# Optimization experiments

Measured on AMD Instinct MI355X. Metric: run time of the kernel, lower is better.

## Reference

```python
import jax, jax.numpy as jnp
import numpy as np

EPS = 1e-5

def _conv(x, w, pad, groups=1):
    return jax.lax.conv_general_dilated(
        x, w, window_strides=(1, 1), padding=[(pad, pad), (pad, pad)],
        dimension_numbers=('NCHW', 'OIHW', 'NCHW'), feature_group_count=groups)

def _bn(x, g, b, m, v):
    # inference batch-norm, per-channel
    s = g * jax.lax.rsqrt(v + EPS)
    return x * s[None, :, None, None] + (b - m * s)[None, :, None, None]

def setup_inputs() -> dict:
    key = jax.random.key(0)
    ks = jax.random.split(key, 20)
    B, C, H, W = 32, 128, 64, 64
    cs = C // 2  # c_split = 64
    d = {
        'x': jax.random.normal(ks[0], (B, C, H, W), jnp.float32),
        'weights': jax.random.uniform(ks[1], (B, 2), jnp.float32),
        'indices': jax.random.randint(ks[2], (B, 2), 0, 4, jnp.int32),
        # expert 0: Conv(cs -> C, k=3, p=1) + BN + SiLU
        'e0_w': jax.random.normal(ks[3], (C, cs, 3, 3), jnp.float32) * 0.05,
        'e0_g': jax.random.uniform(ks[4], (C,), jnp.float32, 0.5, 1.5),
        'e0_b': jax.random.normal(ks[5], (C,), jnp.float32) * 0.1,
        'e0_m': jax.random.normal(ks[6], (C,), jnp.float32) * 0.1,
        'e0_v': jax.random.uniform(ks[7], (C,), jnp.float32, 0.5, 1.5),
        # expert 1: depthwise 5x5 (cs, groups=cs) -> 1x1 (cs -> C) -> BN -> SiLU
        'e1_dw': jax.random.normal(ks[8], (cs, 1, 5, 5), jnp.float32) * 0.05,
        'e1_pw': jax.random.normal(ks[9], (C, cs, 1, 1), jnp.float32) * 0.05,
        'e1_g': jax.random.uniform(ks[10], (C,), jnp.float32, 0.5, 1.5),
        'e1_b': jax.random.normal(ks[11], (C,), jnp.float32) * 0.1,
        'e1_m': jax.random.normal(ks[12], (C,), jnp.float32) * 0.1,
        'e1_v': jax.random.uniform(ks[13], (C,), jnp.float32, 0.5, 1.5),
        # expert 2: GhostConv(C -> C): cv1 = Conv(C, C//2, 3), cv2 = Conv(C//2, C//2, 5, groups=C//2)
        'e2a_w': jax.random.normal(ks[14], (cs, C, 3, 3), jnp.float32) * 0.05,
        'e2a_g': jax.random.uniform(ks[15], (cs,), jnp.float32, 0.5, 1.5),
        'e2a_b': jax.random.normal(ks[16], (cs,), jnp.float32) * 0.1,
        'e2a_m': jax.random.normal(ks[17], (cs,), jnp.float32) * 0.1,
        'e2a_v': jax.random.uniform(ks[18], (cs,), jnp.float32, 0.5, 1.5),
        'e2b_w': jax.random.normal(ks[19], (cs, 1, 5, 5), jnp.float32) * 0.05,
    }
    ks2 = jax.random.split(jax.random.key(1), 4)
    d['e2b_g'] = jax.random.uniform(ks2[0], (cs,), jnp.float32, 0.5, 1.5)
    d['e2b_b'] = jax.random.normal(ks2[1], (cs,), jnp.float32) * 0.1
    d['e2b_m'] = jax.random.normal(ks2[2], (cs,), jnp.float32) * 0.1
    d['e2b_v'] = jax.random.uniform(ks2[3], (cs,), jnp.float32, 0.5, 1.5)
    return d

def _forward(x, weights, indices,
             e0_w, e0_g, e0_b, e0_m, e0_v,
             e1_dw, e1_pw, e1_g, e1_b, e1_m, e1_v,
             e2a_w, e2a_g, e2a_b, e2a_m, e2a_v,
             e2b_w, e2b_g, e2b_b, e2b_m, e2b_v):
    C = x.shape[1]
    cs = C // 2
    x_rgb, x_ir = x[:, :cs], x[:, cs:]
    # expert outputs computed densely over the whole batch, masked combine below
    e0 = jax.nn.silu(_bn(_conv(x_rgb, e0_w, pad=1), e0_g, e0_b, e0_m, e0_v))
    e1 = jax.nn.silu(_bn(_conv(_conv(x_ir, e1_dw, pad=2, groups=cs), e1_pw, pad=0),
                         e1_g, e1_b, e1_m, e1_v))
    g1 = jax.nn.silu(_bn(_conv(x, e2a_w, pad=1), e2a_g, e2a_b, e2a_m, e2a_v))
    g2 = jax.nn.silu(_bn(_conv(g1, e2b_w, pad=2, groups=cs), e2b_g, e2b_b, e2b_m, e2b_v))
    e2 = jnp.concatenate([g1, g2], axis=1)
    out = jnp.zeros_like(x)
    K = indices.shape[1]
    for k in range(K):  # small fixed top-k loop
        idx = indices[:, k][:, None, None, None]          # [B,1,1,1]
        w = weights[:, k][:, None, None, None]            # [B,1,1,1]
        out = out + jnp.where(idx == 0, e0 * w, 0.0)
        out = out + jnp.where(idx == 1, e1 * w, 0.0)
        out = out + jnp.where(idx == 2, e2 * w, 0.0)
        out = out + jnp.where(idx == 3, x * 0.1, 0.0)
    return out

def reference(x, weights, indices,
              e0_w, e0_g, e0_b, e0_m, e0_v,
              e1_dw, e1_pw, e1_g, e1_b, e1_m, e1_v,
              e2a_w, e2a_g, e2a_b, e2a_m, e2a_v,
              e2b_w, e2b_g, e2b_b, e2b_m, e2b_v):
    return _forward(x, weights, indices,
                    e0_w, e0_g, e0_b, e0_m, e0_v,
                    e1_dw, e1_pw, e1_g, e1_b, e1_m, e1_v,
                    e2a_w, e2a_g, e2a_b, e2a_m, e2a_v,
                    e2b_w, e2b_g, e2b_b, e2b_m, e2b_v)
```

## Files before the change

kernel.cpp:

```cpp
#include <hip/hip_runtime.h>

#define B_  32
#define C_  128
#define CS  64
#define H_  64
#define W_  64
#define HW  (H_*W_)

typedef __attribute__((ext_vector_type(8))) short bf16x8_t;
typedef __attribute__((ext_vector_type(4))) float f32x4_t;
typedef unsigned short u16;
typedef unsigned int   u32;

__device__ __forceinline__ float silu_f(float v) { return v / (1.f + __expf(-v)); }

__device__ __forceinline__ u16 f2bf(float f) {
    u32 u = __float_as_uint(f);
    u = (u + 0x7FFFu + ((u >> 16) & 1u)) >> 16;
    return (u16)u;
}
__device__ __forceinline__ float bf2f(u16 u) {
    return __uint_as_float(((u32)u) << 16);
}
__device__ __forceinline__ u32 pack2(float a, float b) {
    return (u32)f2bf(a) | ((u32)f2bf(b) << 16);
}

__device__ __forceinline__ void get_coeffs(const float* __restrict__ wts,
                                           const int* __restrict__ idxs, int b,
                                           float& c0, float& c1, float& c2, float& cid) {
    int   i0 = idxs[b*2+0], i1 = idxs[b*2+1];
    float w0 = wts[b*2+0],  w1 = wts[b*2+1];
    c0  = (i0==0?w0:0.f)   + (i1==0?w1:0.f);
    c1  = (i0==1?w0:0.f)   + (i1==1?w1:0.f);
    c2  = (i0==2?w0:0.f)   + (i1==2?w1:0.f);
    cid = (i0==3?0.1f:0.f) + (i1==3?0.1f:0.f);
}

__global__ __launch_bounds__(256) void k_prep(
    const float* __restrict__ e0w, const float* __restrict__ e2aw, const float* __restrict__ e1pw,
    u16* __restrict__ Wt0f, u16* __restrict__ Wt2f, u16* __restrict__ Wt1f)
{
    const int i0 = blockIdx.x*256 + threadIdx.x, stride = gridDim.x*256;
    for (int i = i0; i < 73728; i += stride) {
        int j = i&7, lane = (i>>3)&63, cog = (i>>9)&7, kc = (i>>12)&1, tap = i>>13;
        int co = cog*16 + (lane&15), ci = kc*32 + (lane>>4)*8 + j;
        Wt0f[i] = f2bf(e0w[(size_t)(co*64 + ci)*9 + tap]);
    }
    for (int i = i0; i < 73728; i += stride) {
        int j = i&7, lane = (i>>3)&63, cog = (i>>9)&3, kc = (i>>11)&3, tap = i>>13;
        int co = cog*16 + (lane&15), ci = kc*32 + (lane>>4)*8 + j;
        Wt2f[i] = f2bf(e2aw[(size_t)(co*128 + ci)*9 + tap]);
    }
    for (int i = i0; i < 8192; i += stride) {
        int j = i&7, lane = (i>>3)&63, cog = (i>>9)&7, kc = (i>>12)&1;
        int co = cog*16 + (lane&15), ci = kc*32 + (lane>>4)*8 + j;
        Wt1f[i] = f2bf(e1pw[(size_t)co*64 + ci]);
    }
}

__global__ __launch_bounds__(256) void k_to_nhwc(
    const float* __restrict__ x, const float* __restrict__ wts, const int* __restrict__ idxs,
    u16* __restrict__ xhA, u16* __restrict__ xhB)
{
    const int b = blockIdx.y, h = blockIdx.x, t = threadIdx.x;
    float c0, c1, c2, cid;
    get_coeffs(wts, idxs, b, c0, c1, c2, cid);
    if (c0 == 0.f && c2 == 0.f) return;
    const int np = (c2 != 0.f) ? 2 : 1;
    const int chmax = np*64;

    __shared__ float ld[128*66];
    for (int i = t; i < chmax*16; i += 256) {
        int ch = i >> 4, q = i & 15;
        float4 v = *(const float4*)(x + ((size_t)(b*C_+ch))*HW + h*64 + q*4);
        float* p = &ld[ch*66 + q*4];
        p[0] = v.x; p[1] = v.y; p[2] = v.z; p[3] = v.w;
    }
    __syncthreads();

    const int px = t >> 2, sub = t & 3;
    const size_t base64 = ((size_t)(b*66 + h+1)*66 + (px+1))*64;
    for (int c = sub; c < chmax/8; c += 4) {
        uint4 v;
        u32 w[4];
        #pragma unroll
        for (int k = 0; k < 4; ++k)
            w[k] = pack2(ld[(c*8 + 2*k)*66 + px], ld[(c*8 + 2*k + 1)*66 + px]);
        v.x = w[0]; v.y = w[1]; v.z = w[2]; v.w = w[3];
        u16* dst = (c < 8) ? (xhA + base64 + c*8) : (xhB + base64 + (c-8)*8);
        *(uint4*)dst = v;
    }
    for (int i = t; i < 16*np; i += 256) {
        int pl = i >> 4, j = i & 15;
        int col = (j >> 3)*65, cg = j & 7;
        u16* ph = pl ? xhB : xhA;
        uint4 z; z.x = z.y = z.z = z.w = 0u;
        *(uint4*)(ph + ((size_t)(b*66 + h+1)*66 + col)*64 + cg*8) = z;
    }
    if (h == 0 || h == 63) {
        int r = (h == 0) ? 0 : 65;
        for (int i = t; i < 66*8*np; i += 256) {
            int pl = i / (66*8), j = i % (66*8);
            int col = j >> 3, cg = j & 7;
            u16* ph = pl ? xhB : xhA;
            uint4 z; z.x = z.y = z.z = z.w = 0u;
            *(uint4*)(ph + ((size_t)(b*66 + r)*64*66/64*64 + (size_t)col*64) + cg*8) = z;
        }
    }
}

template<int MODE>
__device__ __forceinline__ void conv_body(
    u16* lin, const u16* __restrict__ xhA, const u16* __restrict__ xhB,
    const float* __restrict__ x, const u16* __restrict__ Wtf,
    const float* __restrict__ gg, const float* __restrict__ bbn,
    const float* __restrict__ mm, const float* __restrict__ vv,
    float* __restrict__ out, u16* __restrict__ g1,
    int b, int orow0, int t, float cexp, float cid)
{
    constexpr int NPL  = (MODE == 0) ? 1 : 2;
    constexpr int NCF  = (MODE == 0) ? 4 : 2;
    constexpr int COUT = (MODE == 0) ? 128 : 64;
    constexpr int KCT  = (MODE == 0) ? 2 : 4;
    constexpr int NIT  = 9*KCT;

    const size_t src0 = ((size_t)(b*66 + orow0))*66*64;
    #pragma unroll
    for (int pl = 0; pl < NPL; ++pl) {
        const u16* sp = (pl ? xhB : xhA) + src0;
        char* lp = ((char*)lin) + pl*33792;
        for (int d = t*16; d < 33792; d += 4096) {
            u32 s = (u32)d ^ ((((u32)d >> 7) & 7u) << 4);
            *(uint4*)(lp + d) = *(const uint4*)((const char*)sp + s);
        }
    }
    __syncthreads();

    const int lane = t & 63, l15 = lane & 15, kg = lane >> 4;
    const int wv = t >> 6, cw = wv >> 1, rw = wv & 1;
    const int cobase = cw * (NCF*16);
    const int row = orow0 + rw;

    f32x4_t acc[NCF][4];
    #pragma unroll
    for (int cf = 0; cf < NCF; ++cf)
        #pragma unroll
        for (int pf = 0; pf < 4; ++pf)
            acc[cf][pf] = (f32x4_t){0.f, 0.f, 0.f, 0.f};

    const u16* wb = Wtf + (size_t)(cobase >> 4)*512 + (size_t)lane*8;

    bf16x8_t aC[NCF], aN[NCF];
    auto loadA = [&](int it, bf16x8_t* a) {
        const u16* wt = wb + (size_t)(it*(COUT/16))*512;
        #pragma unroll
        for (int cf = 0; cf < NCF; ++cf)
            a[cf] = *(const bf16x8_t*)(wt + (cf << 9));
    };
    auto ldsB = [&](int it, int pf) -> bf16x8_t {
        const int tap = it / KCT, kcg = it % KCT;
        const int pl = (MODE == 0) ? 0 : (kcg >> 1);
        const int kc = (MODE == 0) ? kcg : (kcg & 1);
        const int dh = tap / 3, dwp = tap % 3;
        const int p  = (rw + dh)*66 + pf*16 + l15 + dwp;
        u32 a = (u32)p*128 + (u32)kc*64 + (u32)kg*16;
        a ^= ((u32)(p & 7)) << 4;
        return *(const bf16x8_t*)(((const char*)lin) + pl*33792 + a);
    };

    loadA(0, aC);
    #pragma unroll
    for (int it = 0; it < NIT; ++it) {
        bf16x8_t* ac = (it & 1) ? aN : aC;
        bf16x8_t* an = (it & 1) ? aC : aN;
        if (it + 1 < NIT) loadA(it + 1, an);
        bf16x8_t bfr[4];
        #pragma unroll
        for (int pf = 0; pf < 4; ++pf) bfr[pf] = ldsB(it, pf);
        #pragma unroll
        for (int pf = 0; pf < 4; ++pf)
            #pragma unroll
            for (int cf = 0; cf < NCF; ++cf)
                acc[cf][pf] = __builtin_amdgcn_mfma_f32_16x16x32_bf16(ac[cf], bfr[pf], acc[cf][pf], 0, 0, 0);
    }

    #pragma unroll
    for (int cf = 0; cf < NCF; ++cf) {
        float sarr[4], tarr[4];
        #pragma unroll
        for (int r = 0; r < 4; ++r) {
            int co = cobase + cf*16 + kg*4 + r;
            float s = gg[co] * rsqrtf(vv[co] + 1e-5f);
            sarr[r] = s; tarr[r] = bbn[co] - mm[co]*s;
        }
        #pragma unroll
        for (int pf = 0; pf < 4; ++pf) {
            int px = pf*16 + l15;
            size_t rowoff = (size_t)row*64 + px;
            #pragma unroll
            for (int r = 0; r < 4; ++r) {
                int co = cobase + cf*16 + kg*4 + r;
                float v = silu_f(acc[cf][pf][r]*sarr[r] + tarr[r]);
                if (MODE == 0) {
                    size_t o = ((size_t)(b*C_+co))*HW + rowoff;
                    float idv = (cid != 0.f) ? cid*x[o] : 0.f;
                    out[o] = cexp*v + idv;
                } else {
                    g1[((size_t)(b*CS+co))*HW + rowoff] = f2bf(v);
                }
            }
        }
    }
}

__global__ __launch_bounds__(256, 3) void k_conv(
    const u16* __restrict__ xhA, const u16* __restrict__ xhB, const float* __restrict__ x,
    const float* __restrict__ wts, const int* __restrict__ idxs,
    const u16* __restrict__ Wt0f, const u16* __restrict__ Wt2f,
    const float* __restrict__ e0g, const float* __restrict__ e0b,
    const float* __restrict__ e0m, const float* __restrict__ e0v,
    const float* __restrict__ e2ag, const float* __restrict__ e2ab,
    const float* __restrict__ e2am, const float* __restrict__ e2av,
    float* __restrict__ out, u16* __restrict__ g1)
{
    __shared__ u16 lin[2*16896];
    const int b = blockIdx.y, bx = blockIdx.x, t = threadIdx.x;
    float c0, c1, c2, cid;
    get_coeffs(wts, idxs, b, c0, c1, c2, cid);

    if (bx < 32) {
        const int orow0 = bx*2;
        if (c0 == 0.f) {
            for (int i = t; i < 4096; i += 256) {
                int q = i & 15, r = (i >> 4) & 1, ch = i >> 5;
                size_t o = ((size_t)(b*C_+ch))*HW + (size_t)(orow0+r)*64 + q*4;
                float4 ov;
                if (cid != 0.f) {
                    float4 xv = *(const float4*)(x + o);
                    ov.x = cid*xv.x; ov.y = cid*xv.y; ov.z = cid*xv.z; ov.w = cid*xv.w;
                } else { ov.x = ov.y = ov.z = ov.w = 0.f; }
                *(float4*)(out + o) = ov;
            }
            return;
        }
        conv_body<0>(lin, xhA, xhB, x, Wt0f, e0g, e0b, e0m, e0v, out, nullptr,
                     b, orow0, t, c0, cid);
    } else {
        if (c2 == 0.f) return;
        conv_body<1>(lin, xhA, xhB, x, Wt2f, e2ag, e2ab, e2am, e2av, nullptr, g1,
                     b, (bx-32)*2, t, c2, 0.f);
    }
}

__global__ __launch_bounds__(256) void k_e1(
    const float* __restrict__ x, const float* __restrict__ wts, const int* __restrict__ idxs,
    const float* __restrict__ dww, const u16* __restrict__ Wt1f,
    const float* __restrict__ gg, const float* __restrict__ bb,
    const float* __restrict__ mm, const float* __restrict__ vv,
    float* __restrict__ out)
{
    const int b = blockIdx.y, band = blockIdx.x, t = threadIdx.x;
    const int orow0 = band*2;

    float c0, c1, c2, cid;
    get_coeffs(wts, idxs, b, c0, c1, c2, cid);
    if (c1 == 0.f) return;

    __shared__ u16  lin[6*64*70];
    __shared__ u16  lout[128*72];
    __shared__ float wl[64*26];

    for (int i = t; i < 64*25; i += 256) wl[(i/25)*26 + (i%25)] = dww[i];
    for (int i = t; i < 6*64*16; i += 256) {
        int q = i & 15, ch = (i >> 4) & 63, r = i >> 10;
        int hh = orow0 - 2 + r;
        u32 w0 = 0u, w1 = 0u;
        if (hh >= 0 && hh < H_) {
            float4 v = *(const float4*)(x + ((size_t)(b*C_ + CS + ch))*HW + hh*64 + q*4);
            w0 = pack2(v.x, v.y); w1 = pack2(v.z, v.w);
        }
        u32* dst = (u32*)&lin[(r*64 + ch)*70 + 2 + q*4];
        dst[0] = w0; dst[1] = w1;
    }
    for (int i = t; i < 6*64; i += 256) {
        int ch = i & 63, r = i >> 6;
        *(u32*)&lin[(r*64 + ch)*70]      = 0u;
        u32* e = (u32*)&lin[(r*64 + ch)*70 + 66];
        e[0] = 0u; e[1] = 0u;
    }
    __syncthreads();

    const int lane = t & 63, chl = lane & 15, cs = lane >> 4;
    const int wv = t >> 6, outrow = wv & 1, chhalf = wv >> 1;

    #pragma unroll
    for (int chi = 0; chi < 2; ++chi) {
        const int ch = chhalf*32 + chl + chi*16;
        const float* wch = &wl[ch*26];
        float accp[16];
        #pragma unroll
        for (int p = 0; p < 16; ++p) accp[p] = 0.f;
        #pragma unroll
        for (int kh = 0; kh < 5; ++kh) {
            const u16* src = &lin[((outrow + kh)*64 + ch)*70 + cs*16];
            float rb[20];
            #pragma unroll
            for (int k = 0; k < 10; ++k) {
                u32 u = *(const u32*)(src + 2*k);
                rb[2*k]   = __uint_as_float(u << 16);
                rb[2*k+1] = __uint_as_float(u & 0xFFFF0000u);
            }
            #pragma unroll
            for (int kw = 0; kw < 5; ++kw) {
                float wvv = wch[kh*5 + kw];
                #pragma unroll
                for (int p = 0; p < 16; ++p) accp[p] += rb[p+kw]*wvv;
            }
        }
        const int px0 = outrow*64 + cs*16;
        #pragma unroll
        for (int p = 0; p < 16; ++p) lout[(px0+p)*72 + ch] = f2bf(accp[p]);
    }
    __syncthreads();

    const int l15 = lane & 15, kg = lane >> 4;
    const int cw = wv >> 1, pwv = wv & 1;
    f32x4_t acc[4][4];
    #pragma unroll
    for (int cf = 0; cf < 4; ++cf)
        #pragma unroll
        for (int pf = 0; pf < 4; ++pf)
            acc[cf][pf] = (f32x4_t){0.f, 0.f, 0.f, 0.f};

    #pragma unroll
    for (int kc = 0; kc < 2; ++kc) {
        const u16* wt = Wt1f + (((size_t)(kc*8 + cw*4)) << 9) + lane*8;
        bf16x8_t af[4];
        #pragma unroll
        for (int cf = 0; cf < 4; ++cf) af[cf] = *(const bf16x8_t*)(wt + (cf << 9));
        const int k0 = kc*32 + kg*8;
        #pragma unroll
        for (int pf = 0; pf < 4; ++pf) {
            bf16x8_t bfr = *(const bf16x8_t*)&lout[(pwv*64 + pf*16 + l15)*72 + k0];
            #pragma unroll
            for (int cf = 0; cf < 4; ++cf)
                acc[cf][pf] = __builtin_amdgcn_mfma_f32_16x16x32_bf16(af[cf], bfr, acc[cf][pf], 0, 0, 0);
        }
    }

    #pragma unroll
    for (int cf = 0; cf < 4; ++cf) {
        float sarr[4], tarr[4];
        #pragma unroll
        for (int r = 0; r < 4; ++r) {
            int co = cw*64 + cf*16 + kg*4 + r;
            float s = gg[co] * rsqrtf(vv[co] + 1e-5f);
            sarr[r] = s; tarr[r] = bb[co] - mm[co]*s;
        }
        #pragma unroll
        for (int pf = 0; pf < 4; ++pf) {
            int px = pwv*64 + pf*16 + l15;
            size_t rowoff = (size_t)(orow0 + (px>>6))*64 + (px&63);
            #pragma unroll
            for (int r = 0; r < 4; ++r) {
                int co = cw*64 + cf*16 + kg*4 + r;
                float v = silu_f(acc[cf][pf][r]*sarr[r] + tarr[r]);
                out[((size_t)(b*C_+co))*HW + rowoff] += c1*v;
            }
        }
    }
}

__global__ __launch_bounds__(256) void k_e2b(
    const u16* __restrict__ g1, const float* __restrict__ wts, const int* __restrict__ idxs,
    const float* __restrict__ dww, const float* __restrict__ gg, const float* __restrict__ bb,
    const float* __restrict__ mm, const float* __restrict__ vv, float* __restrict__ out)
{
    const int b = blockIdx.y, band = blockIdx.x, t = threadIdx.x;
    const int orow0 = band*2;

    float c0, c1, c2, cid;
    get_coeffs(wts, idxs, b, c0, c1, c2, cid);
    if (c2 == 0.f) return;

    __shared__ u16  lin[6*64*70];
    __shared__ float wl[64*26];

    for (int i = t; i < 64*25; i += 256) wl[(i/25)*26 + (i%25)] = dww[i];
    for (int i = t; i < 6*64*16; i += 256) {
        int q = i & 15, ch = (i >> 4) & 63, r = i >> 10;
        int hh = orow0 - 2 + r;
        u32 w0 = 0u, w1 = 0u;
        if (hh >= 0 && hh < H_) {
            const u32* src = (const u32*)(g1 + ((size_t)(b*CS+ch))*HW + hh*64 + q*4);
            w0 = src[0]; w1 = src[1];
        }
        u32* dst = (u32*)&lin[(r*64 + ch)*70 + 2 + q*4];
        dst[0] = w0; dst[1] = w1;
    }
    for (int i = t; i < 6*64; i += 256) {
        int ch = i & 63, r = i >> 6;
        *(u32*)&lin[(r*64 + ch)*70] = 0u;
        u32* e = (u32*)&lin[(r*64 + ch)*70 + 66];
        e[0] = 0u; e[1] = 0u;
    }
    __syncthreads();

    for (int i = t; i < 2*64*16; i += 256) {
        int q = i & 15, ch = (i >> 4) & 63, r = i >> 10;
        const u16* src = &lin[((r+2)*64 + ch)*70 + 2 + q*4];
        float* op = out + ((size_t)(b*C_+ch))*HW + (size_t)(orow0+r)*64 + q*4;
        float4 ov = *(float4*)op;
        ov.x += c2*bf2f(src[0]); ov.y += c2*bf2f(src[1]);
        ov.z += c2*bf2f(src[2]); ov.w += c2*bf2f(src[3]);
        *(float4*)op = ov;
    }

    const int lane = t & 63, chl = lane & 15, cs = lane >> 4;
    const int wv = t >> 6, outrow = wv & 1, chhalf = wv >> 1;

    #pragma unroll
    for (int chi = 0; chi < 2; ++chi) {
        const int ch = chhalf*32 + chl + chi*16;
        const float* wch = &wl[ch*26];
        float accp[16];
        #pragma unroll
        for (int p = 0; p < 16; ++p) accp[p] = 0.f;
        #pragma unroll
        for (int kh = 0; kh < 5; ++kh) {
            const u16* src = &lin[((outrow + kh)*64 + ch)*70 + cs*16];
            float rb[20];
            #pragma unroll
            for (int k = 0; k < 10; ++k) {
                u32 u = *(const u32*)(src + 2*k);
                rb[2*k]   = __uint_as_float(u << 16);
                rb[2*k+1] = __uint_as_float(u & 0xFFFF0000u);
            }
            #pragma unroll
            for (int kw = 0; kw < 5; ++kw) {
                float wvv = wch[kh*5 + kw];
                #pragma unroll
                for (int p = 0; p < 16; ++p) accp[p] += rb[p+kw]*wvv;
            }
        }
        float s = gg[ch] * rsqrtf(vv[ch] + 1e-5f);
        float tt = bb[ch] - mm[ch]*s;
        float* op = out + ((size_t)(b*C_ + CS + ch))*HW + (size_t)(orow0+outrow)*64 + cs*16;
        #pragma unroll
        for (int q = 0; q < 4; ++q) {
            float4 ov = *(float4*)(op + q*4);
            ov.x += c2*silu_f(accp[q*4+0]*s + tt);
            ov.y += c2*silu_f(accp[q*4+1]*s + tt);
            ov.z += c2*silu_f(accp[q*4+2]*s + tt);
            ov.w += c2*silu_f(accp[q*4+3]*s + tt);
            *(float4*)(op + q*4) = ov;
        }
    }
}

extern "C" void kernel_launch(void* const* d_in, const int* in_sizes, int n_in,
                              void* d_out, int out_size, void* d_ws, size_t ws_size,
                              hipStream_t stream) {
    const float* x    = (const float*)d_in[0];
    const float* wts  = (const float*)d_in[1];
    const int*   idxs = (const int*)  d_in[2];
    const float* e0w  = (const float*)d_in[3];
    const float* e0g  = (const float*)d_in[4];
    const float* e0b  = (const float*)d_in[5];
    const float* e0m  = (const float*)d_in[6];
    const float* e0v  = (const float*)d_in[7];
    const float* e1dw = (const float*)d_in[8];
    const float* e1pw = (const float*)d_in[9];
    const float* e1g  = (const float*)d_in[10];
    const float* e1b  = (const float*)d_in[11];
    const float* e1m  = (const float*)d_in[12];
    const float* e1v  = (const float*)d_in[13];
    const float* e2aw = (const float*)d_in[14];
    const float* e2ag = (const float*)d_in[15];
    const float* e2ab = (const float*)d_in[16];
    const float* e2am = (const float*)d_in[17];
    const float* e2av = (const float*)d_in[18];
    const float* e2bw = (const float*)d_in[19];
    const float* e2bg = (const float*)d_in[20];
    const float* e2bb = (const float*)d_in[21];
    const float* e2bm = (const float*)d_in[22];
    const float* e2bv = (const float*)d_in[23];

    float* out = (float*)d_out;

    const size_t PLANE = (size_t)32*66*66*64;
    u16* xhA  = (u16*)d_ws;
    u16* xhB  = xhA + PLANE;
    u16* g1   = xhB + PLANE;
    u16* Wt0f = g1 + (size_t)8388608;
    u16* Wt2f = Wt0f + 73728;
    u16* Wt1f = Wt2f + 73728;

    k_prep<<<128, 256, 0, stream>>>(e0w, e2aw, e1pw, Wt0f, Wt2f, Wt1f);
    k_to_nhwc<<<dim3(64, B_), 256, 0, stream>>>(x, wts, idxs, xhA, xhB);
    k_conv<<<dim3(64, B_), 256, 0, stream>>>(
        xhA, xhB, x, wts, idxs, Wt0f, Wt2f,
        e0g, e0b, e0m, e0v, e2ag, e2ab, e2am, e2av, out, g1);
    k_e1<<<dim3(32, B_), 256, 0, stream>>>(
        x, wts, idxs, e1dw, Wt1f, e1g, e1b, e1m, e1v, out);
    k_e2b<<<dim3(32, B_), 256, 0, stream>>>(
        g1, wts, idxs, e2bw, e2bg, e2bb, e2bm, e2bv, out);
}
```

Baseline: 116.0 us.

## Merge expert-0 and GhostConv-cv1 convolutions into one block sharing staged input

Expert 0 and the GhostConv first conv previously ran in separate blocks that each staged the same input band into LDS. They now run in one block per two-row band: waves 0-1 compute the 128-channel expert-0 conv over both rows, and waves 2-3 compute the 64-channel cv1 conv, one row each. The change removes redundant global-to-LDS loads of the shared xhA plane and halves the grid. In exchange each wave holds more accumulators, occupancy drops to 2 blocks per SM, and the work is split unevenly between the two wave pairs. It also fixes the halo-row zero-fill address expression.

```diff
diff --git a/kernel.cpp b/kernel.cpp
--- a/kernel.cpp
+++ b/kernel.cpp
@@ -105,48 +105,27 @@
             int col = j >> 3, cg = j & 7;
             u16* ph = pl ? xhB : xhA;
             uint4 z; z.x = z.y = z.z = z.w = 0u;
-            *(uint4*)(ph + ((size_t)(b*66 + r)*64*66/64*64 + (size_t)col*64) + cg*8) = z;
-        }
-    }
-}
-
-template<int MODE>
-__device__ __forceinline__ void conv_body(
-    u16* lin, const u16* __restrict__ xhA, const u16* __restrict__ xhB,
-    const float* __restrict__ x, const u16* __restrict__ Wtf,
+            *(uint4*)(ph + ((size_t)(b*66 + r)*66 + (size_t)col)*64 + cg*8) = z;
+        }
+    }
+}
+
+template<int NCF, int NPF, int KCT, int COUT, int MODE>
+__device__ __forceinline__ void conv_wave(
+    const char* lin, const u16* __restrict__ Wtf,
     const float* __restrict__ gg, const float* __restrict__ bbn,
     const float* __restrict__ mm, const float* __restrict__ vv,
-    float* __restrict__ out, u16* __restrict__ g1,
-    int b, int orow0, int t, float cexp, float cid)
+    const float* __restrict__ x, float* __restrict__ out, u16* __restrict__ g1,
+    int b, int orow0, int rbase, int cobase, int lane, float cexp, float cid)
 {
-    constexpr int NPL  = (MODE == 0) ? 1 : 2;
-    constexpr int NCF  = (MODE == 0) ? 4 : 2;
-    constexpr int COUT = (MODE == 0) ? 128 : 64;
-    constexpr int KCT  = (MODE == 0) ? 2 : 4;
-    constexpr int NIT  = 9*KCT;
-
-    const size_t src0 = ((size_t)(b*66 + orow0))*66*64;
-    #pragma unroll
-    for (int pl = 0; pl < NPL; ++pl) {
-        const u16* sp = (pl ? xhB : xhA) + src0;
-        char* lp = ((char*)lin) + pl*33792;
-        for (int d = t*16; d < 33792; d += 4096) {
-            u32 s = (u32)d ^ ((((u32)d >> 7) & 7u) << 4);
-            *(uint4*)(lp + d) = *(const uint4*)((const char*)sp + s);
-        }
-    }
-    __syncthreads();
-
-    const int lane = t & 63, l15 = lane & 15, kg = lane >> 4;
-    const int wv = t >> 6, cw = wv >> 1, rw = wv & 1;
-    const int cobase = cw * (NCF*16);
-    const int row = orow0 + rw;
-
-    f32x4_t acc[NCF][4];
+    constexpr int NIT = 9*KCT;
+    const int l15 = lane & 15, kg = lane >> 4;
+
+    f32x4_t acc[NCF][NPF];
     #pragma unroll
     for (int cf = 0; cf < NCF; ++cf)
         #pragma unroll
-        for (int pf = 0; pf < 4; ++pf)
+        for (int pf = 0; pf < NPF; ++pf)
             acc[cf][pf] = (f32x4_t){0.f, 0.f, 0.f, 0.f};
 
     const u16* wb = Wtf + (size_t)(cobase >> 4)*512 + (size_t)lane*8;
@@ -160,13 +139,14 @@
     };
     auto ldsB = [&](int it, int pf) -> bf16x8_t {
         const int tap = it / KCT, kcg = it % KCT;
-        const int pl = (MODE == 0) ? 0 : (kcg >> 1);
-        const int kc = (MODE == 0) ? kcg : (kcg & 1);
+        const int pl = kcg >> 1, kc = kcg & 1;
         const int dh = tap / 3, dwp = tap % 3;
-        const int p  = (rw + dh)*66 + pf*16 + l15 + dwp;
+        const int prow = (NPF == 8) ? (pf >> 2) : rbase;
+        const int pcol = (NPF == 8) ? ((pf & 3)*16) : (pf*16);
+        const int p = (prow + dh)*66 + pcol + l15 + dwp;
         u32 a = (u32)p*128 + (u32)kc*64 + (u32)kg*16;
         a ^= ((u32)(p & 7)) << 4;
-        return *(const bf16x8_t*)(((const char*)lin) + pl*33792 + a);
+        return *(const bf16x8_t*)(lin + pl*33792 + a);
     };
 
     loadA(0, aC);
@@ -175,14 +155,13 @@
         bf16x8_t* ac = (it & 1) ? aN : aC;
         bf16x8_t* an = (it & 1) ? aC : aN;
         if (it + 1 < NIT) loadA(it + 1, an);
-        bf16x8_t bfr[4];
-        #pragma unroll
-        for (int pf = 0; pf < 4; ++pf) bfr[pf] = ldsB(it, pf);
-        #pragma unroll
-        for (int pf = 0; pf < 4; ++pf)
+        #pragma unroll
+        for (int pf = 0; pf < NPF; ++pf) {
+            bf16x8_t bfr = ldsB(it, pf);
             #pragma unroll
             for (int cf = 0; cf < NCF; ++cf)
-                acc[cf][pf] = __builtin_amdgcn_mfma_f32_16x16x32_bf16(ac[cf], bfr[pf], acc[cf][pf], 0, 0, 0);
+                acc[cf][pf] = __builtin_amdgcn_mfma_f32_16x16x32_bf16(ac[cf], bfr, acc[cf][pf], 0, 0, 0);
+        }
     }
 
     #pragma unroll
@@ -195,9 +174,10 @@
             sarr[r] = s; tarr[r] = bbn[co] - mm[co]*s;
         }
         #pragma unroll
-        for (int pf = 0; pf < 4; ++pf) {
-            int px = pf*16 + l15;
-            size_t rowoff = (size_t)row*64 + px;
+        for (int pf = 0; pf < NPF; ++pf) {
+            const int prow = (NPF == 8) ? (pf >> 2) : rbase;
+            const int pcol = (NPF == 8) ? ((pf & 3)*16) : (pf*16);
+            size_t rowoff = (size_t)(orow0 + prow)*64 + pcol + l15;
             #pragma unroll
             for (int r = 0; r < 4; ++r) {
                 int co = cobase + cf*16 + kg*4 + r;
@@ -214,7 +194,7 @@
     }
 }
 
-__global__ __launch_bounds__(256, 3) void k_conv(
+__global__ __launch_bounds__(256, 2) void k_conv(
     const u16* __restrict__ xhA, const u16* __restrict__ xhB, const float* __restrict__ x,
     const float* __restrict__ wts, const int* __restrict__ idxs,
     const u16* __restrict__ Wt0f, const u16* __restrict__ Wt2f,
@@ -224,17 +204,51 @@
     const float* __restrict__ e2am, const float* __restrict__ e2av,
     float* __restrict__ out, u16* __restrict__ g1)
 {
-    __shared__ u16 lin[2*16896];
-    const int b = blockIdx.y, bx = blockIdx.x, t = threadIdx.x;
+    __shared__ char lin[2*33792];
+    const int b = blockIdx.y, orow0 = blockIdx.x*2, t = threadIdx.x;
     float c0, c1, c2, cid;
     get_coeffs(wts, idxs, b, c0, c1, c2, cid);
-
-    if (bx < 32) {
-        const int orow0 = bx*2;
-        if (c0 == 0.f) {
-            for (int i = t; i < 4096; i += 256) {
-                int q = i & 15, r = (i >> 4) & 1, ch = i >> 5;
-                size_t o = ((size_t)(b*C_+ch))*HW + (size_t)(orow0+r)*64 + q*4;
+    const bool need0 = (c0 != 0.f), need2 = (c2 != 0.f);
+
+    if (!need0 && !need2) {
+        for (int i = t; i < 4096; i += 256) {
+            int ch = i >> 5, q = i & 31;
+            size_t o = ((size_t)(b*C_+ch))*HW + (size_t)orow0*64 + q*4;
+            float4 ov;
+            if (cid != 0.f) {
+                float4 xv = *(const float4*)(x + o);
+                ov.x = cid*xv.x; ov.y = cid*xv.y; ov.z = cid*xv.z; ov.w = cid*xv.w;
+            } else { ov.x = ov.y = ov.z = ov.w = 0.f; }
+            *(float4*)(out + o) = ov;
+        }
+        return;
+    }
+
+    {
+        const size_t src0 = ((size_t)(b*66 + orow0))*66*64;
+        for (int d = t*16; d < 33792; d += 4096) {
+            u32 s = (u32)d ^ ((((u32)d >> 7) & 7u) << 4);
+            *(uint4*)(lin + d) = *(const uint4*)((const char*)(xhA + src0) + s);
+        }
+        if (need2) {
+            for (int d = t*16; d < 33792; d += 4096) {
+                u32 s = (u32)d ^ ((((u32)d >> 7) & 7u) << 4);
+                *(uint4*)(lin + 33792 + d) = *(const uint4*)((const char*)(xhB + src0) + s);
+            }
+        }
+    }
+    __syncthreads();
+
+    const int wv = t >> 6, lane = t & 63;
+    if (wv < 2) {
+        if (need0) {
+            conv_wave<4, 8, 2, 128, 0>(lin, Wt0f, e0g, e0b, e0m, e0v, x, out, nullptr,
+                                       b, orow0, 0, wv*64, lane, c0, cid);
+        } else {
+            for (int k = 0; k < 32; ++k) {
+                int idx = k*64 + lane;
+                int ch = wv*64 + (idx >> 5), q = idx & 31;
+                size_t o = ((size_t)(b*C_+ch))*HW + (size_t)orow0*64 + q*4;
                 float4 ov;
                 if (cid != 0.f) {
                     float4 xv = *(const float4*)(x + o);
@@ -242,14 +256,11 @@
                 } else { ov.x = ov.y = ov.z = ov.w = 0.f; }
                 *(float4*)(out + o) = ov;
             }
-            return;
-        }
-        conv_body<0>(lin, xhA, xhB, x, Wt0f, e0g, e0b, e0m, e0v, out, nullptr,
-                     b, orow0, t, c0, cid);
+        }
     } else {
-        if (c2 == 0.f) return;
-        conv_body<1>(lin, xhA, xhB, x, Wt2f, e2ag, e2ab, e2am, e2av, nullptr, g1,
-                     b, (bx-32)*2, t, c2, 0.f);
+        if (need2)
+            conv_wave<4, 4, 4, 64, 1>(lin, Wt2f, e2ag, e2ab, e2am, e2av, x, nullptr, g1,
+                                      b, orow0, wv - 2, 0, lane, c2, 0.f);
     }
 }
 
@@ -499,7 +510,7 @@
 
     k_prep<<<128, 256, 0, stream>>>(e0w, e2aw, e1pw, Wt0f, Wt2f, Wt1f);
     k_to_nhwc<<<dim3(64, B_), 256, 0, stream>>>(x, wts, idxs, xhA, xhB);
-    k_conv<<<dim3(64, B_), 256, 0, stream>>>(
+    k_conv<<<dim3(32, B_), 256, 0, stream>>>(
         xhA, xhB, x, wts, idxs, Wt0f, Wt2f,
         e0g, e0b, e0m, e0v, e2ag, e2ab, e2am, e2av, out, g1);
     k_e1<<<dim3(32, B_), 256, 0, stream>>>(
```

After: 134.3 us. 1.16x slower.

## Halve conv LDS footprint by staging GhostConv input planes sequentially

Applied to the files above, without the earlier changes.

Cuts the k_conv shared buffer from two staged input planes to one. The GhostConv cv1 path now stages plane A, accumulates, then restages plane B. Its waves are also re-split into 4 row/pixel groups that each cover all 64 output channels, and launch bounds rise to 4 blocks per CU for higher occupancy. The grid now uses a z dimension to pick the branch. The cost is an extra barrier and restaging pass in the e2a branch, plus possible register pressure at the higher occupancy target.

```diff
diff --git a/kernel.cpp b/kernel.cpp
--- a/kernel.cpp
+++ b/kernel.cpp
@@ -105,116 +105,51 @@
             int col = j >> 3, cg = j & 7;
             u16* ph = pl ? xhB : xhA;
             uint4 z; z.x = z.y = z.z = z.w = 0u;
-            *(uint4*)(ph + ((size_t)(b*66 + r)*64*66/64*64 + (size_t)col*64) + cg*8) = z;
-        }
-    }
-}
-
-template<int MODE>
-__device__ __forceinline__ void conv_body(
-    u16* lin, const u16* __restrict__ xhA, const u16* __restrict__ xhB,
-    const float* __restrict__ x, const u16* __restrict__ Wtf,
-    const float* __restrict__ gg, const float* __restrict__ bbn,
-    const float* __restrict__ mm, const float* __restrict__ vv,
-    float* __restrict__ out, u16* __restrict__ g1,
-    int b, int orow0, int t, float cexp, float cid)
+            *(uint4*)(ph + ((size_t)(b*66 + r)*66 + (size_t)col)*64 + cg*8) = z;
+        }
+    }
+}
+
+template<int NCF, int NPF, int TK, int COUT>
+__device__ __forceinline__ void conv_pass(
+    const char* lin, const u16* __restrict__ wb, int koff,
+    int rbase, int pxbase, int l15, int kg,
+    f32x4_t (&acc)[NCF][NPF])
 {
-    constexpr int NPL  = (MODE == 0) ? 1 : 2;
-    constexpr int NCF  = (MODE == 0) ? 4 : 2;
-    constexpr int COUT = (MODE == 0) ? 128 : 64;
-    constexpr int KCT  = (MODE == 0) ? 2 : 4;
-    constexpr int NIT  = 9*KCT;
-
-    const size_t src0 = ((size_t)(b*66 + orow0))*66*64;
-    #pragma unroll
-    for (int pl = 0; pl < NPL; ++pl) {
-        const u16* sp = (pl ? xhB : xhA) + src0;
-        char* lp = ((char*)lin) + pl*33792;
-        for (int d = t*16; d < 33792; d += 4096) {
-            u32 s = (u32)d ^ ((((u32)d >> 7) & 7u) << 4);
-            *(uint4*)(lp + d) = *(const uint4*)((const char*)sp + s);
-        }
-    }
-    __syncthreads();
-
-    const int lane = t & 63, l15 = lane & 15, kg = lane >> 4;
-    const int wv = t >> 6, cw = wv >> 1, rw = wv & 1;
-    const int cobase = cw * (NCF*16);
-    const int row = orow0 + rw;
-
-    f32x4_t acc[NCF][4];
-    #pragma unroll
-    for (int cf = 0; cf < NCF; ++cf)
-        #pragma unroll
-        for (int pf = 0; pf < 4; ++pf)
-            acc[cf][pf] = (f32x4_t){0.f, 0.f, 0.f, 0.f};
-
-    const u16* wb = Wtf + (size_t)(cobase >> 4)*512 + (size_t)lane*8;
-
     bf16x8_t aC[NCF], aN[NCF];
-    auto loadA = [&](int it, bf16x8_t* a) {
-        const u16* wt = wb + (size_t)(it*(COUT/16))*512;
+    auto loadA = [&](int i, bf16x8_t* a) {
+        const int tap = i >> 1, kcl = i & 1;
+        const u16* wt = wb + (size_t)((tap*TK + koff + kcl)*(COUT/16))*512;
         #pragma unroll
         for (int cf = 0; cf < NCF; ++cf)
             a[cf] = *(const bf16x8_t*)(wt + (cf << 9));
     };
-    auto ldsB = [&](int it, int pf) -> bf16x8_t {
-        const int tap = it / KCT, kcg = it % KCT;
-        const int pl = (MODE == 0) ? 0 : (kcg >> 1);
-        const int kc = (MODE == 0) ? kcg : (kcg & 1);
+    auto ldsB = [&](int i, int pf) -> bf16x8_t {
+        const int tap = i >> 1, kcl = i & 1;
         const int dh = tap / 3, dwp = tap % 3;
-        const int p  = (rw + dh)*66 + pf*16 + l15 + dwp;
-        u32 a = (u32)p*128 + (u32)kc*64 + (u32)kg*16;
+        const int p = (rbase + dh)*66 + pxbase + pf*16 + l15 + dwp;
+        u32 a = (u32)p*128 + (u32)kcl*64 + (u32)kg*16;
         a ^= ((u32)(p & 7)) << 4;
-        return *(const bf16x8_t*)(((const char*)lin) + pl*33792 + a);
+        return *(const bf16x8_t*)(lin + a);
     };
 
     loadA(0, aC);
     #pragma unroll
-    for (int it = 0; it < NIT; ++it) {
-        bf16x8_t* ac = (it & 1) ? aN : aC;
-        bf16x8_t* an = (it & 1) ? aC : aN;
-        if (it + 1 < NIT) loadA(it + 1, an);
-        bf16x8_t bfr[4];
-        #pragma unroll
-        for (int pf = 0; pf < 4; ++pf) bfr[pf] = ldsB(it, pf);
-        #pragma unroll
-        for (int pf = 0; pf < 4; ++pf)
+    for (int i = 0; i < 18; ++i) {
+        bf16x8_t* ac = (i & 1) ? aN : aC;
+        bf16x8_t* an = (i & 1) ? aC : aN;
+        if (i + 1 < 18) loadA(i + 1, an);
+        #pragma unroll
+        for (int pf = 0; pf < NPF; ++pf) {
+            bf16x8_t bfr = ldsB(i, pf);
             #pragma unroll
             for (int cf = 0; cf < NCF; ++cf)
-                acc[cf][pf] = __builtin_amdgcn_mfma_f32_16x16x32_bf16(ac[cf], bfr[pf], acc[cf][pf], 0, 0, 0);
-    }
-
-    #pragma unroll
-    for (int cf = 0; cf < NCF; ++cf) {
-        float sarr[4], tarr[4];
-        #pragma unroll
-        for (int r = 0; r < 4; ++r) {
-            int co = cobase + cf*16 + kg*4 + r;
-            float s = gg[co] * rsqrtf(vv[co] + 1e-5f);
-            sarr[r] = s; tarr[r] = bbn[co] - mm[co]*s;
-        }
-        #pragma unroll
-        for (int pf = 0; pf < 4; ++pf) {
-            int px = pf*16 + l15;
-            size_t rowoff = (size_t)row*64 + px;
-            #pragma unroll
-            for (int r = 0; r < 4; ++r) {
-                int co = cobase + cf*16 + kg*4 + r;
-                float v = silu_f(acc[cf][pf][r]*sarr[r] + tarr[r]);
-                if (MODE == 0) {
-                    size_t o = ((size_t)(b*C_+co))*HW + rowoff;
-                    float idv = (cid != 0.f) ? cid*x[o] : 0.f;
-                    out[o] = cexp*v + idv;
-                } else {
-                    g1[((size_t)(b*CS+co))*HW + rowoff] = f2bf(v);
-                }
-            }
-        }
-    }
-}
-
-__global__ __launch_bounds__(256, 3) void k_conv(
+                acc[cf][pf] = __builtin_amdgcn_mfma_f32_16x16x32_bf16(ac[cf], bfr, acc[cf][pf], 0, 0, 0);
+        }
+    }
+}
+
+__global__ __launch_bounds__(256, 4) void k_conv(
     const u16* __restrict__ xhA, const u16* __restrict__ xhB, const float* __restrict__ x,
     const float* __restrict__ wts, const int* __restrict__ idxs,
     const u16* __restrict__ Wt0f, const u16* __restrict__ Wt2f,
@@ -224,17 +159,27 @@
     const float* __restrict__ e2am, const float* __restrict__ e2av,
     float* __restrict__ out, u16* __restrict__ g1)
 {
-    __shared__ u16 lin[2*16896];
-    const int b = blockIdx.y, bx = blockIdx.x, t = threadIdx.x;
+    __shared__ char lin[33792];
+    const int b = blockIdx.y, orow0 = blockIdx.x*2, t = threadIdx.x;
     float c0, c1, c2, cid;
     get_coeffs(wts, idxs, b, c0, c1, c2, cid);
 
-    if (bx < 32) {
-        const int orow0 = bx*2;
+    const int lane = t & 63, l15 = lane & 15, kg = lane >> 4, wv = t >> 6;
+    const size_t src0 = ((size_t)(b*66 + orow0))*66*64;
+
+    auto stage = [&](const u16* src) {
+        const char* sp = (const char*)src;
+        for (int d = t*16; d < 33792; d += 4096) {
+            u32 s = (u32)d ^ ((((u32)d >> 7) & 7u) << 4);
+            *(uint4*)(lin + d) = *(const uint4*)(sp + s);
+        }
+    };
+
+    if (blockIdx.z == 0) {
         if (c0 == 0.f) {
             for (int i = t; i < 4096; i += 256) {
-                int q = i & 15, r = (i >> 4) & 1, ch = i >> 5;
-                size_t o = ((size_t)(b*C_+ch))*HW + (size_t)(orow0+r)*64 + q*4;
+                int ch = i >> 5, q = i & 31;
+                size_t o = ((size_t)(b*C_+ch))*HW + (size_t)orow0*64 + q*4;
                 float4 ov;
                 if (cid != 0.f) {
                     float4 xv = *(const float4*)(x + o);
@@ -244,12 +189,85 @@
             }
             return;
         }
-        conv_body<0>(lin, xhA, xhB, x, Wt0f, e0g, e0b, e0m, e0v, out, nullptr,
-                     b, orow0, t, c0, cid);
+        stage(xhA + src0);
+        __syncthreads();
+
+        const int cw = wv >> 1, rw = wv & 1;
+        const int cobase = cw*64;
+        f32x4_t acc[4][4];
+        #pragma unroll
+        for (int cf = 0; cf < 4; ++cf)
+            #pragma unroll
+            for (int pf = 0; pf < 4; ++pf)
+                acc[cf][pf] = (f32x4_t){0.f, 0.f, 0.f, 0.f};
+
+        const u16* wb = Wt0f + (size_t)(cobase >> 4)*512 + (size_t)lane*8;
+        conv_pass<4, 4, 2, 128>(lin, wb, 0, rw, 0, l15, kg, acc);
+
+        #pragma unroll
+        for (int cf = 0; cf < 4; ++cf) {
+            float sarr[4], tarr[4];
+            #pragma unroll
+            for (int r = 0; r < 4; ++r) {
+                int co = cobase + cf*16 + kg*4 + r;
+                float s = e0g[co] * rsqrtf(e0v[co] + 1e-5f);
+                sarr[r] = s; tarr[r] = e0b[co] - e0m[co]*s;
+            }
+            #pragma unroll
+            for (int pf = 0; pf < 4; ++pf) {
+                size_t rowoff = (size_t)(orow0 + rw)*64 + pf*16 + l15;
+                #pragma unroll
+                for (int r = 0; r < 4; ++r) {
+                    int co = cobase + cf*16 + kg*4 + r;
+                    float v = silu_f(acc[cf][pf][r]*sarr[r] + tarr[r]);
+                    size_t o = ((size_t)(b*C_+co))*HW + rowoff;
+                    float idv = (cid != 0.f) ? cid*x[o] : 0.f;
+                    out[o] = c0*v + idv;
+                }
+            }
+        }
     } else {
         if (c2 == 0.f) return;
-        conv_body<1>(lin, xhA, xhB, x, Wt2f, e2ag, e2ab, e2am, e2av, nullptr, g1,
-                     b, (bx-32)*2, t, c2, 0.f);
+
+        const int rw = wv >> 1, pw = wv & 1;
+        const int pxbase = pw*32;
+        f32x4_t acc[4][2];
+        #pragma unroll
+        for (int cf = 0; cf < 4; ++cf)
+            #pragma unroll
+            for (int pf = 0; pf < 2; ++pf)
+                acc[cf][pf] = (f32x4_t){0.f, 0.f, 0.f, 0.f};
+
+        const u16* wb = Wt2f + (size_t)lane*8;
+
+        stage(xhA + src0);
+        __syncthreads();
+        conv_pass<4, 2, 4, 64>(lin, wb, 0, rw, pxbase, l15, kg, acc);
+        __syncthreads();
+        stage(xhB + src0);
+        __syncthreads();
+        conv_pass<4, 2, 4, 64>(lin, wb, 2, rw, pxbase, l15, kg, acc);
+
+        #pragma unroll
+        for (int cf = 0; cf < 4; ++cf) {
+            float sarr[4], tarr[4];
+            #pragma unroll
+            for (int r = 0; r < 4; ++r) {
+                int co = cf*16 + kg*4 + r;
+                float s = e2ag[co] * rsqrtf(e2av[co] + 1e-5f);
+                sarr[r] = s; tarr[r] = e2ab[co] - e2am[co]*s;
+            }
+            #pragma unroll
+            for (int pf = 0; pf < 2; ++pf) {
+                size_t rowoff = (size_t)(orow0 + rw)*64 + pxbase + pf*16 + l15;
+                #pragma unroll
+                for (int r = 0; r < 4; ++r) {
+                    int co = cf*16 + kg*4 + r;
+                    float v = silu_f(acc[cf][pf][r]*sarr[r] + tarr[r]);
+                    g1[((size_t)(b*CS+co))*HW + rowoff] = f2bf(v);
+                }
+            }
+        }
     }
 }
 
@@ -499,7 +517,7 @@
 
     k_prep<<<128, 256, 0, stream>>>(e0w, e2aw, e1pw, Wt0f, Wt2f, Wt1f);
     k_to_nhwc<<<dim3(64, B_), 256, 0, stream>>>(x, wts, idxs, xhA, xhB);
-    k_conv<<<dim3(64, B_), 256, 0, stream>>>(
+    k_conv<<<dim3(32, B_, 2), 256, 0, stream>>>(
         xhA, xhB, x, wts, idxs, Wt0f, Wt2f,
         e0g, e0b, e0m, e0v, e2ag, e2ab, e2am, e2av, out, g1);
     k_e1<<<dim3(32, B_), 256, 0, stream>>>(
```

New measurement: 110.8 us. 1.05x faster.
